# Optimization experiments

Measured on AMD Instinct MI355X. Metric: run time of the kernel, lower is better.

The kernel has to match this reference:

```python
import jax, jax.numpy as jnp
import numpy as np

B, N, H, V = 2048, 16, 512, 780  # trees, nodes per tree, hidden size, vocab size


def _topology():
    """Build one random tree, replicate across B trees, and precompute the
    BFS level schedule on the non-backtracking line graph (as DGL's
    level_order: reversed(edges_back) = up edges leaves-first, then
    edges = down edges root-first)."""
    rng = np.random.default_rng(0)
    parent = np.zeros(N, dtype=np.int64)
    for i in range(1, N):
        parent[i] = rng.integers(0, i)
    depth = np.zeros(N, dtype=np.int64)
    for i in range(1, N):
        depth[i] = depth[parent[i]] + 1
    Epc = 2 * (N - 1)  # directed edges per tree
    src = np.zeros(Epc, dtype=np.int64)
    dst = np.zeros(Epc, dtype=np.int64)
    for i in range(1, N):
        src[2 * (i - 1)] = parent[i]; dst[2 * (i - 1)] = i          # down edge
        src[2 * (i - 1) + 1] = i;     dst[2 * (i - 1) + 1] = parent[i]  # up edge
    # line-graph predecessors of edge e=(u->v): edges f=(w->u) with w != v
    preds = [[f for f in range(Epc) if dst[f] == src[e] and src[f] != dst[e]]
             for e in range(Epc)]
    P = max(1, max(len(p) for p in preds))
    preds_pad = np.full((Epc, P), -1, dtype=np.int64)
    for e, p in enumerate(preds):
        preds_pad[e, :len(p)] = p
    D = int(depth.max())
    levels = []
    for d in range(D, 0, -1):   # upward pass, deepest level first
        levels.append([2 * (i - 1) + 1 for i in range(1, N) if depth[i] == d])
    for d in range(1, D + 1):   # downward pass, root first
        levels.append([2 * (i - 1) for i in range(1, N) if depth[i] == d])
    E = B * Epc                 # index E is the zero dummy row
    offs = np.arange(B, dtype=np.int64) * Epc
    preds_full = np.where(preds_pad[None] >= 0,
                          preds_pad[None] + offs[:, None, None], E)
    preds_full = preds_full.reshape(E, P)
    preds_full = np.concatenate(
        [preds_full, np.full((1, P), E, dtype=np.int64)], axis=0)  # [E+1, P]
    Mmax = max(len(lv) for lv in levels) * B
    lv_arr = np.full((len(levels), Mmax), E, dtype=np.int64)
    for l, lv in enumerate(levels):
        ids = (np.asarray(lv, np.int64)[None] + offs[:, None]).reshape(-1)
        lv_arr[l, :ids.size] = ids
    edge_src = (src[None] + np.arange(B, dtype=np.int64)[:, None] * N).reshape(-1)
    root_children = [2 * (i - 1) + 1 for i in range(1, N) if parent[i] == 0]
    root_in = np.asarray(root_children, np.int64)[None] + offs[:, None]  # [B, R]
    root_nodes = np.arange(B, dtype=np.int64) * N
    return edge_src, preds_full, lv_arr, root_in, root_nodes


def setup_inputs() -> dict:
    key = jax.random.key(0)
    ks = jax.random.split(key, 11)
    edge_src, preds, levels, root_in, root_nodes = _topology()
    s1 = 1.0 / np.sqrt(H)
    s2 = 1.0 / np.sqrt(2 * H)
    return {
        "wid": jax.random.randint(ks[0], (B * N,), 0, V),
        "edge_src": jnp.asarray(edge_src),
        "preds": jnp.asarray(preds),
        "levels": jnp.asarray(levels),
        "root_in": jnp.asarray(root_in),
        "root_nodes": jnp.asarray(root_nodes),
        "emb": jax.random.normal(ks[1], (V, H), jnp.float32),
        "w_r": jax.random.normal(ks[2], (H, H), jnp.float32) * s1,
        "ur_w": jax.random.normal(ks[3], (H, H), jnp.float32) * s1,
        "ur_b": jax.random.normal(ks[4], (H,), jnp.float32) * s1,
        "wz_w": jax.random.normal(ks[5], (2 * H, H), jnp.float32) * s2,
        "wz_b": jax.random.normal(ks[6], (H,), jnp.float32) * s2,
        "wh_w": jax.random.normal(ks[7], (2 * H, H), jnp.float32) * s2,
        "wh_b": jax.random.normal(ks[8], (H,), jnp.float32) * s2,
        "wo_w": jax.random.normal(ks[9], (2 * H, H), jnp.float32) * s2,
        "wo_b": jax.random.normal(ks[10], (H,), jnp.float32) * s2,
    }


def reference(wid, edge_src, preds, levels, root_in, root_nodes,
              emb, w_r, ur_w, ur_b, wz_w, wz_b, wh_w, wh_b, wo_w, wo_b):
    E = edge_src.shape[0]
    Hd = emb.shape[1]
    x = emb[wid]                                           # [B*N, H]
    zero = jnp.zeros((1, Hd), x.dtype)
    sx_all = x[edge_src]                                   # src_x per edge
    src_x = jnp.concatenate([sx_all, zero], axis=0)        # [E+1, H], row E = 0
    src_x_r = jnp.concatenate([sx_all @ w_r, zero], axis=0)  # W_r (no bias)
    h = jnp.zeros((E + 1, Hd), x.dtype)
    for l in range(levels.shape[0]):                       # static BFS levels
        idx = levels[l]                                    # [M], padded with E
        p = preds[idx]                                     # [M, P]
        h_nei = h[p]                                       # [M, P, H]
        sum_h = h_nei.sum(axis=1)
        # GRUMessage: r = sigmoid(dst.src_x_r + U_r(src.h)); m = r * src.h
        r = jax.nn.sigmoid(src_x_r[idx][:, None, :] + h_nei @ ur_w + ur_b)
        sum_g = (r * h_nei).sum(axis=1)
        sx = src_x[idx]
        # GRUUpdate
        z = jax.nn.sigmoid(jnp.concatenate([sx, sum_h], axis=-1) @ wz_w + wz_b)
        pre_h = jnp.tanh(jnp.concatenate([sx, sum_g], axis=-1) @ wh_w + wh_b)
        h = h.at[idx].set((1.0 - z) * sum_h + z * pre_h)
        h = h.at[E].set(0.0)                               # keep dummy row zero
    h_edges = h[:E]                                        # edata['h']
    h_root = h[root_in].sum(axis=1)                        # pull into roots
    x_root = x[root_nodes]
    root_vec = jax.nn.relu(
        jnp.concatenate([x_root, h_root], axis=-1) @ wo_w + wo_b)
    return h_edges, root_vec
```

## Files before the change

kernel.cpp:

```cpp
#include <hip/hip_runtime.h>
#include <hip/hip_bf16.h>
#include <cstddef>

#define HD 512

typedef short s8v __attribute__((ext_vector_type(8)));
typedef short s4v __attribute__((ext_vector_type(4)));
typedef float fx4 __attribute__((ext_vector_type(4)));

#define MFMA(a, b, c) __builtin_amdgcn_mfma_f32_16x16x32_bf16((a), (b), (c), 0, 0, 0)

__device__ __forceinline__ unsigned short f2bf(float f) {
  unsigned int u = __float_as_uint(f);
  unsigned int r = (u + 0x7fffu + ((u >> 16) & 1u)) >> 16;
  return (unsigned short)r;
}
__device__ __forceinline__ float bf2f(unsigned short u) {
  return __uint_as_float(((unsigned int)u) << 16);
}

__device__ __forceinline__ size_t swz_off(int k, int n, int KT) {
  int kt = k >> 5, kr = k & 31;
  int nt = n >> 4, nr = n & 15;
  int lane = ((kr >> 3) << 4) | nr;
  int i = kr & 7;
  return ((((size_t)nt * KT + kt) * 64 + lane) << 3) + i;
}

__global__ void pack_kernel(const float* w_r, const float* ur, const float* wz, const float* wh,
                            const float* wo,
                            unsigned short* W1, unsigned short* WZB, unsigned short* WHB,
                            unsigned short* WUR, unsigned short* WO) {
  int idx = blockIdx.x * blockDim.x + threadIdx.x;
  int stride = gridDim.x * blockDim.x;
  for (int t = idx; t < 512 * 1536; t += stride) {
    int k = t / 1536, n = t - k * 1536;
    float v;
    if (n < 512) v = w_r[k * 512 + n];
    else if (n < 1024) v = wz[k * 512 + (n - 512)];
    else v = wh[k * 512 + (n - 1024)];
    W1[swz_off(k, n, 16)] = f2bf(v);
  }
  for (int t = idx; t < 512 * 512; t += stride) {
    int k = t >> 9, n = t & 511;
    size_t o = swz_off(k, n, 16);
    WZB[o] = f2bf(wz[(512 + k) * 512 + n]);
    WHB[o] = f2bf(wh[(512 + k) * 512 + n]);
    WUR[o] = f2bf(ur[k * 512 + n]);
  }
  for (int t = idx; t < 1024 * 512; t += stride) {
    int k = t >> 9, n = t & 511;
    WO[swz_off(k, n, 32)] = f2bf(wo[k * 512 + n]);
  }
}

__global__ void embed_kernel(const int* wid, const float* emb, unsigned short* x_bf, int BN) {
  int idx = blockIdx.x * blockDim.x + threadIdx.x;
  int stride = gridDim.x * blockDim.x;
  int total = BN * (HD / 8);
  for (int t = idx; t < total; t += stride) {
    int nrow = t >> 6;
    int c8 = (t & 63) << 3;
    int w = wid[nrow];
    const float4* s = (const float4*)(emb + (size_t)w * HD + c8);
    float4 v0 = s[0], v1 = s[1];
    s8v o;
    o[0] = (short)f2bf(v0.x); o[1] = (short)f2bf(v0.y);
    o[2] = (short)f2bf(v0.z); o[3] = (short)f2bf(v0.w);
    o[4] = (short)f2bf(v1.x); o[5] = (short)f2bf(v1.y);
    o[6] = (short)f2bf(v1.z); o[7] = (short)f2bf(v1.w);
    *(s8v*)&x_bf[(size_t)nrow * HD + c8] = o;
  }
}

__global__ void schedule_kernel(const int* preds, int E, int Epc, int P, int* sched) {
  __shared__ int rnd[64];
  int t = threadIdx.x;
  rnd[t] = -1;
  __syncthreads();
  for (int it = 0; it <= Epc; ++it) {
    int newv = -1;
    if (t < Epc && rnd[t] < 0) {
      int mx = 0;
      bool ready = true;
      for (int q = 0; q < P; ++q) {
        int pe = preds[t * P + q];
        if (pe < E) {
          int rp = rnd[pe];
          if (rp < 0) ready = false;
          else if (rp + 1 > mx) mx = rp + 1;
        }
      }
      if (ready) newv = mx;
    }
    __syncthreads();
    if (newv >= 0) rnd[t] = newv;
    __syncthreads();
  }
  if (t == 0) {
    int R = 0;
    for (int e = 0; e < Epc; ++e) if (rnd[e] + 1 > R) R = rnd[e] + 1;
    if (R > 31) R = 31;
    sched[0] = R;
    for (int r = 0; r < 31; ++r) {
      int c = 0;
      if (r < R) {
        for (int e = 0; e < Epc; ++e) if (rnd[e] == r) { sched[33 + r * 32 + c] = e; ++c; }
      }
      sched[1 + r] = c;
    }
  }
}

__global__ __launch_bounds__(512, 4) void gemm_pre_kernel(const unsigned short* x_bf,
                                                          const unsigned short* W1,
                                                          unsigned short* XP, int BN) {
  __shared__ unsigned short lA[2][128 * 72];
  const int nM = BN >> 7;
  const int slab = blockIdx.x / nM;
  const int mt = blockIdx.x - slab * nM;
  const int tid = threadIdx.x, lane = tid & 63, w = tid >> 6;
  const int wm = w & 1, wn = w >> 1;
  const int m0 = mt << 7;
  const int srow = tid >> 2, sc0 = (tid & 3) << 4;
  const int k8 = (lane >> 4) << 3;
  fx4 ac[16];
#pragma unroll
  for (int i = 0; i < 16; i++) { ac[i][0]=0.f; ac[i][1]=0.f; ac[i][2]=0.f; ac[i][3]=0.f; }
  const unsigned short* aptr = x_bf + (size_t)(m0 + srow) * 512 + sc0;
  s8v r0, r1;
  {
    r0 = *(const s8v*)aptr;
    r1 = *(const s8v*)(aptr + 8);
    *(s8v*)&lA[0][srow * 72 + sc0]     = r0;
    *(s8v*)&lA[0][srow * 72 + sc0 + 8] = r1;
    r0 = *(const s8v*)(aptr + 64);
    r1 = *(const s8v*)(aptr + 72);
  }
  for (int ks = 0; ks < 8; ++ks) {
    const int cur = ks & 1;
    __syncthreads();
    if (ks < 7) {
      *(s8v*)&lA[cur ^ 1][srow * 72 + sc0]     = r0;
      *(s8v*)&lA[cur ^ 1][srow * 72 + sc0 + 8] = r1;
    }
    if (ks < 6) {
      const unsigned short* g = aptr + ((ks + 2) << 6);
      r0 = *(const s8v*)g;
      r1 = *(const s8v*)(g + 8);
    }
#pragma unroll
    for (int sub = 0; sub < 2; ++sub) {
      const int kt = (ks << 1) + sub;
      s8v a[4];
#pragma unroll
      for (int mi = 0; mi < 4; ++mi)
        a[mi] = *(const s8v*)&lA[cur][((wm << 6) + (mi << 4) + (lane & 15)) * 72 + (sub << 5) + k8];
#pragma unroll
      for (int ni = 0; ni < 4; ++ni) {
        const int ntile = (slab << 4) + (wn << 2) + ni;
        const s8v b = *(const s8v*)(W1 + ((((size_t)ntile << 4) + kt) * 64 + lane) * 8);
#pragma unroll
        for (int mi = 0; mi < 4; ++mi) ac[mi * 4 + ni] = MFMA(a[mi], b, ac[mi * 4 + ni]);
      }
    }
  }
#pragma unroll
  for (int mi = 0; mi < 4; ++mi) {
#pragma unroll
    for (int q = 0; q < 4; ++q) {
      const int row = (wm << 6) + (mi << 4) + ((lane >> 4) << 2) + q;
#pragma unroll
      for (int ni = 0; ni < 4; ++ni) {
        const int col = (slab << 8) + (wn << 6) + (ni << 4) + (lane & 15);
        XP[(size_t)(m0 + row) * 1536 + col] = f2bf(ac[mi * 4 + ni][q]);
      }
    }
  }
}

struct AP {
  const int* sched;
  const int* preds;
  const int* edge_src;
  const float* ur_b;
  const unsigned short* XP;
  const unsigned short* u_bf_c;
  const unsigned short* hE_c;
  unsigned short* A2h;
  unsigned short* A2g;
  int* eIdx;
  int* srcIdx;
  int B, Epc, P, E;
};

__global__ __launch_bounds__(256) void gatherA_kernel(AP p, int r) {
  const int cnt = p.sched[1 + r];
  if (cnt == 0) return;
  const int M = cnt * p.B;
  const int* lst = p.sched + 33 + r * 32;
  const int lane = threadIdx.x & 63;
  const int waveId = blockIdx.x * 4 + (threadIdx.x >> 6);
  const int totalWaves = gridDim.x * 4;
  for (int m = waveId; m < M; m += totalWaves) {
    const int b = m / cnt;
    const int j = m - b * cnt;
    const int e = b * p.Epc + lst[j];
    const int src = p.edge_src[e];
    if (lane == 0) { p.eIdx[m] = e; p.srcIdx[m] = src; }
    const int c0 = lane << 3;
    const s8v xr8 = *(const s8v*)&p.XP[(size_t)src * 1536 + c0];
    float xb[8], ub[8], sh[8], sg[8];
#pragma unroll
    for (int i = 0; i < 8; i++) {
      xb[i] = bf2f((unsigned short)xr8[i]);
      ub[i] = p.ur_b[c0 + i];
      sh[i] = 0.f; sg[i] = 0.f;
    }
    for (int t = 0; t < p.P; ++t) {
      const int pe = p.preds[(size_t)e * p.P + t];
      if (pe >= p.E) continue;
      const s8v h8 = *(const s8v*)&p.hE_c[(size_t)pe * 512 + c0];
      const s8v u8 = *(const s8v*)&p.u_bf_c[(size_t)pe * 512 + c0];
#pragma unroll
      for (int i = 0; i < 8; i++) {
        const float hv = bf2f((unsigned short)h8[i]);
        const float rr = 1.f / (1.f + __expf(-(xb[i] + bf2f((unsigned short)u8[i]) + ub[i])));
        sh[i] += hv;
        sg[i] += rr * hv;
      }
    }
    s8v shb, sgb;
#pragma unroll
    for (int i = 0; i < 8; i++) { shb[i] = (short)f2bf(sh[i]); sgb[i] = (short)f2bf(sg[i]); }
    *(s8v*)&p.A2h[(size_t)m * 512 + c0] = shb;
    *(s8v*)&p.A2g[(size_t)m * 512 + c0] = sgb;
  }
}

struct BP {
  const int* sched;
  const float* wz_b;
  const float* wh_b;
  const unsigned short* XP;
  const unsigned short* A2h;
  const unsigned short* A2g;
  const unsigned short* WZB;
  const unsigned short* WHB;
  const int* eIdx;
  const int* srcIdx;
  unsigned short* hE;
  int B;
};

__global__ __launch_bounds__(256, 4) void gemmB_kernel(BP p, int r) {
  const int cnt = p.sched[1 + r];
  if (cnt == 0) return;
  const int M = cnt * p.B;
  const int nT = (M >> 5) << 1;
  const int qq = nT >> 3;
  __shared__ unsigned short lZ[2][32 * 72];
  __shared__ unsigned short lH[2][32 * 72];
  __shared__ int eL[32];
  __shared__ int sL[32];
  const int tid = threadIdx.x, lane = tid & 63, w = tid >> 6;
  const int srow = tid >> 3, sc = (tid & 7) << 3;
  const int k8 = (lane >> 4) << 3;

  for (int t0 = blockIdx.x; t0 < nT; t0 += gridDim.x) {
    const int t = (t0 & 7) * qq + (t0 >> 3);
    const int mt = t >> 1, nb = t & 1;
    const int m0 = mt << 5, n0 = nb << 8;
    if (tid < 32) { eL[tid] = p.eIdx[m0 + tid]; sL[tid] = p.srcIdx[m0 + tid]; }
    fx4 aZ[8], aH[8];
#pragma unroll
    for (int i = 0; i < 8; i++) {
      aZ[i][0]=0.f; aZ[i][1]=0.f; aZ[i][2]=0.f; aZ[i][3]=0.f;
      aH[i][0]=0.f; aH[i][1]=0.f; aH[i][2]=0.f; aH[i][3]=0.f;
    }
    const size_t rbase = (size_t)(m0 + srow) * 512 + sc;
    s8v nh, ng;
    {
      *(s8v*)&lZ[0][srow * 72 + sc] = *(const s8v*)&p.A2h[rbase];
      *(s8v*)&lH[0][srow * 72 + sc] = *(const s8v*)&p.A2g[rbase];
      nh = *(const s8v*)&p.A2h[rbase + 64];
      ng = *(const s8v*)&p.A2g[rbase + 64];
    }
    for (int ks = 0; ks < 8; ++ks) {
      const int cur = ks & 1;
      __syncthreads();
      if (ks < 7) {
        *(s8v*)&lZ[cur ^ 1][srow * 72 + sc] = nh;
        *(s8v*)&lH[cur ^ 1][srow * 72 + sc] = ng;
      }
      if (ks < 6) {
        nh = *(const s8v*)&p.A2h[rbase + ((ks + 2) << 6)];
        ng = *(const s8v*)&p.A2g[rbase + ((ks + 2) << 6)];
      }
#pragma unroll
      for (int sub = 0; sub < 2; ++sub) {
        const int kt = (ks << 1) + sub;
        s8v az[2], ah[2];
#pragma unroll
        for (int mi = 0; mi < 2; ++mi) {
          const int ao = ((mi << 4) + (lane & 15)) * 72 + (sub << 5) + k8;
          az[mi] = *(const s8v*)&lZ[cur][ao];
          ah[mi] = *(const s8v*)&lH[cur][ao];
        }
#pragma unroll
        for (int ni = 0; ni < 4; ++ni) {
          const int ntile = (n0 >> 4) + (w << 2) + ni;
          const size_t boff = ((((size_t)ntile << 4) + kt) * 64 + lane) << 3;
          const s8v bz = *(const s8v*)(p.WZB + boff);
          const s8v bh = *(const s8v*)(p.WHB + boff);
#pragma unroll
          for (int mi = 0; mi < 2; ++mi) {
            aZ[mi * 4 + ni] = MFMA(az[mi], bz, aZ[mi * 4 + ni]);
            aH[mi * 4 + ni] = MFMA(ah[mi], bh, aH[mi * 4 + ni]);
          }
        }
      }
    }
#pragma unroll
    for (int mi = 0; mi < 2; ++mi) {
#pragma unroll
      for (int q4 = 0; q4 < 4; ++q4) {
        const int row = (mi << 4) + ((lane >> 4) << 2) + q4;
        const int e = eL[row];
        const int src = sL[row];
#pragma unroll
        for (int ni = 0; ni < 4; ++ni) {
          const int col = n0 + (w << 6) + (ni << 4) + (lane & 15);
          float zpre = aZ[mi * 4 + ni][q4] + bf2f(p.XP[(size_t)src * 1536 + 512 + col]) + p.wz_b[col];
          float hpre = aH[mi * 4 + ni][q4] + bf2f(p.XP[(size_t)src * 1536 + 1024 + col]) + p.wh_b[col];
          float zz = 1.f / (1.f + __expf(-zpre));
          float e2 = __expf(2.f * hpre);
          float th = 1.f - 2.f / (e2 + 1.f);
          float sumh = bf2f(p.A2h[(size_t)(m0 + row) * 512 + col]);
          float hn = (1.f - zz) * sumh + zz * th;
          p.hE[(size_t)e * 512 + col] = f2bf(hn);
        }
      }
    }
    __syncthreads();
  }
}

struct CP {
  const int* sched;
  const unsigned short* hE;
  const unsigned short* WUR;
  const int* eIdx;
  unsigned short* u_bf;
  int B;
};

__global__ __launch_bounds__(256, 4) void gemmC_kernel(CP p, int r) {
  const int cnt = p.sched[1 + r];
  if (cnt == 0) return;
  const int M = cnt * p.B;
  const int nT = (M >> 5) << 1;
  const int qq = nT >> 3;
  __shared__ unsigned short lA[2][32 * 72];
  __shared__ int eL[32];
  const int tid = threadIdx.x, lane = tid & 63, w = tid >> 6;
  const int srow = tid >> 3, sc = (tid & 7) << 3;
  const int k8 = (lane >> 4) << 3;

  for (int t0 = blockIdx.x; t0 < nT; t0 += gridDim.x) {
    const int t = (t0 & 7) * qq + (t0 >> 3);
    const int mt = t >> 1, nb = t & 1;
    const int m0 = mt << 5, n0 = nb << 8;
    if (tid < 32) eL[tid] = p.eIdx[m0 + tid];
    __syncthreads();
    fx4 ac[8];
#pragma unroll
    for (int i = 0; i < 8; i++) { ac[i][0]=0.f; ac[i][1]=0.f; ac[i][2]=0.f; ac[i][3]=0.f; }
    const unsigned short* gbase = p.hE + (size_t)eL[srow] * 512 + sc;
    s8v ra;
    {
      *(s8v*)&lA[0][srow * 72 + sc] = *(const s8v*)gbase;
      ra = *(const s8v*)(gbase + 64);
    }
    for (int ks = 0; ks < 8; ++ks) {
      const int cur = ks & 1;
      __syncthreads();
      if (ks < 7) {
        *(s8v*)&lA[cur ^ 1][srow * 72 + sc] = ra;
      }
      if (ks < 6) {
        ra = *(const s8v*)(gbase + ((ks + 2) << 6));
      }
#pragma unroll
      for (int sub = 0; sub < 2; ++sub) {
        const int kt = (ks << 1) + sub;
        s8v a[2];
#pragma unroll
        for (int mi = 0; mi < 2; ++mi)
          a[mi] = *(const s8v*)&lA[cur][((mi << 4) + (lane & 15)) * 72 + (sub << 5) + k8];
#pragma unroll
        for (int ni = 0; ni < 4; ++ni) {
          const int ntile = (n0 >> 4) + (w << 2) + ni;
          const size_t boff = ((((size_t)ntile << 4) + kt) * 64 + lane) << 3;
          const s8v bu = *(const s8v*)(p.WUR + boff);
#pragma unroll
          for (int mi = 0; mi < 2; ++mi) ac[mi * 4 + ni] = MFMA(a[mi], bu, ac[mi * 4 + ni]);
        }
      }
    }
#pragma unroll
    for (int mi = 0; mi < 2; ++mi) {
#pragma unroll
      for (int q4 = 0; q4 < 4; ++q4) {
        const int row = (mi << 4) + ((lane >> 4) << 2) + q4;
        const int e = eL[row];
#pragma unroll
        for (int ni = 0; ni < 4; ++ni) {
          const int col = n0 + (w << 6) + (ni << 4) + (lane & 15);
          p.u_bf[(size_t)e * 512 + col] = f2bf(ac[mi * 4 + ni][q4]);
        }
      }
    }
    __syncthreads();
  }
}

__global__ void cvt_kernel(const unsigned short* hE, float* h, int total8) {
  int idx = blockIdx.x * blockDim.x + threadIdx.x;
  int stride = gridDim.x * blockDim.x;
  for (int t = idx; t < total8; t += stride) {
    const s8v v = *(const s8v*)&hE[(size_t)t * 8];
    float4 f0 = make_float4(bf2f((unsigned short)v[0]), bf2f((unsigned short)v[1]),
                            bf2f((unsigned short)v[2]), bf2f((unsigned short)v[3]));
    float4 f1 = make_float4(bf2f((unsigned short)v[4]), bf2f((unsigned short)v[5]),
                            bf2f((unsigned short)v[6]), bf2f((unsigned short)v[7]));
    *(float4*)&h[(size_t)t * 8] = f0;
    *(float4*)&h[(size_t)t * 8 + 4] = f1;
  }
}

__global__ void root_gather_kernel(const int* root_nodes, const int* root_in,
                                   const unsigned short* x_bf, const unsigned short* hE,
                                   unsigned short* Aroot, int B, int R0) {
  int lane = threadIdx.x & 63;
  int waveId = blockIdx.x * (blockDim.x >> 6) + (threadIdx.x >> 6);
  int totalWaves = gridDim.x * (blockDim.x >> 6);
  for (int b = waveId; b < B; b += totalWaves) {
    int c0 = lane << 3;
    int nd = root_nodes[b];
    *(s8v*)&Aroot[(size_t)b * 1024 + c0] = *(const s8v*)&x_bf[(size_t)nd * HD + c0];
    float s[8];
#pragma unroll
    for (int i = 0; i < 8; i++) s[i] = 0.f;
    for (int t = 0; t < R0; ++t) {
      int e = root_in[b * R0 + t];
      const s8v h8 = *(const s8v*)&hE[(size_t)e * 512 + c0];
#pragma unroll
      for (int i = 0; i < 8; i++) s[i] += bf2f((unsigned short)h8[i]);
    }
    s8v sb;
#pragma unroll
    for (int i = 0; i < 8; i++) sb[i] = (short)f2bf(s[i]);
    *(s8v*)&Aroot[(size_t)b * 1024 + 512 + c0] = sb;
  }
}

__global__ __launch_bounds__(256) void gemm_root_kernel(const unsigned short* Aroot,
                                                        const unsigned short* WO,
                                                        const float* wo_b, float* out, int B) {
  __shared__ unsigned short lA[32 * 40];
  int tid = threadIdx.x, lane = tid & 63, w = tid >> 6;
  int wm = w & 1, wn = w >> 1;
  int bt = blockIdx.x;
  int mt = bt >> 1, nt = bt & 1;
  int m0 = mt << 5;
  fx4 ac[8];
#pragma unroll
  for (int n = 0; n < 8; n++) { ac[n][0]=0.f; ac[n][1]=0.f; ac[n][2]=0.f; ac[n][3]=0.f; }
  int srow = tid >> 3, squad = tid & 7;
  int arow = (wm << 4) | (lane & 15), k8 = (lane >> 4) << 3;
  for (int kt = 0; kt < 32; ++kt) {
    const unsigned short* g = Aroot + (size_t)(m0 + srow) * 1024 + (kt << 5) + (squad << 2);
    *(s4v*)&lA[srow * 40 + (squad << 2)] = *(const s4v*)g;
    __syncthreads();
    s8v a = *(const s8v*)&lA[arow * 40 + k8];
#pragma unroll
    for (int n = 0; n < 8; n++) {
      int ntile = (nt << 4) + (wn << 3) + n;
      size_t boff = ((((size_t)ntile * 32) + kt) * 64 + lane) << 3;
      ac[n] = MFMA(a, *(const s8v*)(WO + boff), ac[n]);
    }
    __syncthreads();
  }
#pragma unroll
  for (int q = 0; q < 4; q++) {
    int row = (wm << 4) + ((lane >> 4) << 2) + q;
    int m = m0 + row;
#pragma unroll
    for (int n = 0; n < 8; n++) {
      int col = (nt << 8) + (wn << 7) + (n << 4) + (lane & 15);
      float v = ac[n][q] + wo_b[col];
      out[(size_t)m * HD + col] = v > 0.f ? v : 0.f;
    }
  }
}

extern "C" void kernel_launch(void* const* d_in, const int* in_sizes, int n_in,
                              void* d_out, int out_size, void* d_ws, size_t ws_size,
                              hipStream_t stream) {
  const int* wid = (const int*)d_in[0];
  const int* edge_src = (const int*)d_in[1];
  const int* preds = (const int*)d_in[2];
  const int* root_in = (const int*)d_in[4];
  const int* root_nodes = (const int*)d_in[5];
  const float* emb = (const float*)d_in[6];
  const float* w_r = (const float*)d_in[7];
  const float* ur_w = (const float*)d_in[8];
  const float* ur_b = (const float*)d_in[9];
  const float* wz_w = (const float*)d_in[10];
  const float* wz_b = (const float*)d_in[11];
  const float* wh_w = (const float*)d_in[12];
  const float* wh_b = (const float*)d_in[13];
  const float* wo_w = (const float*)d_in[14];
  const float* wo_b = (const float*)d_in[15];

  const int BN = in_sizes[0];
  const int E = in_sizes[1];
  const int Bt = in_sizes[5];
  const int Epc = E / Bt;
  const int P = in_sizes[2] / (E + 1);
  const int R0 = in_sizes[4] / Bt;

  float* h = (float*)d_out;

  char* wp = (char*)d_ws;
  auto alloc = [&](size_t bytes) {
    char* r = wp;
    wp += (bytes + 255) & ~(size_t)255;
    return r;
  };
  unsigned short* x_bf = (unsigned short*)alloc((size_t)BN * 512 * 2);
  unsigned short* XP = (unsigned short*)alloc((size_t)BN * 1536 * 2);
  unsigned short* u_bf = (unsigned short*)alloc((size_t)E * 512 * 2);
  unsigned short* hE = (unsigned short*)alloc((size_t)E * 512 * 2);
  unsigned short* A2h = (unsigned short*)alloc((size_t)E * 512 * 2);
  unsigned short* A2g = (unsigned short*)alloc((size_t)E * 512 * 2);
  int* eIdx = (int*)alloc((size_t)E * 4);
  int* srcIdx = (int*)alloc((size_t)E * 4);
  unsigned short* W1 = (unsigned short*)alloc((size_t)512 * 1536 * 2);
  unsigned short* WZB = (unsigned short*)alloc((size_t)512 * 512 * 2);
  unsigned short* WHB = (unsigned short*)alloc((size_t)512 * 512 * 2);
  unsigned short* WUR = (unsigned short*)alloc((size_t)512 * 512 * 2);
  unsigned short* WO = (unsigned short*)alloc((size_t)1024 * 512 * 2);
  unsigned short* Aroot = (unsigned short*)alloc((size_t)Bt * 1024 * 2);
  int* sched = (int*)alloc(8192);

  hipLaunchKernelGGL(pack_kernel, dim3(512), dim3(256), 0, stream,
                     w_r, ur_w, wz_w, wh_w, wo_w, W1, WZB, WHB, WUR, WO);
  hipLaunchKernelGGL(embed_kernel, dim3(1024), dim3(256), 0, stream, wid, emb, x_bf, BN);
  hipLaunchKernelGGL(schedule_kernel, dim3(1), dim3(64), 0, stream, preds, E, Epc, P, sched);
  hipLaunchKernelGGL(gemm_pre_kernel, dim3((BN / 128) * 6), dim3(512), 0, stream,
                     x_bf, W1, XP, BN);

  AP ap;
  ap.sched = sched; ap.preds = preds; ap.edge_src = edge_src;
  ap.ur_b = ur_b; ap.XP = XP; ap.u_bf_c = u_bf; ap.hE_c = hE;
  ap.A2h = A2h; ap.A2g = A2g; ap.eIdx = eIdx; ap.srcIdx = srcIdx;
  ap.B = Bt; ap.Epc = Epc; ap.P = P; ap.E = E;

  BP bp;
  bp.sched = sched; bp.wz_b = wz_b; bp.wh_b = wh_b;
  bp.XP = XP; bp.A2h = A2h; bp.A2g = A2g;
  bp.WZB = WZB; bp.WHB = WHB;
  bp.eIdx = eIdx; bp.srcIdx = srcIdx;
  bp.hE = hE; bp.B = Bt;

  CP cp;
  cp.sched = sched; cp.hE = hE; cp.WUR = WUR;
  cp.eIdx = eIdx; cp.u_bf = u_bf; cp.B = Bt;

  for (int r = 0; r < Epc && r < 31; ++r) {
    const int g = (r < 16) ? 1024 : 128;
    hipLaunchKernelGGL(gatherA_kernel, dim3(g), dim3(256), 0, stream, ap, r);
    hipLaunchKernelGGL(gemmB_kernel, dim3(g), dim3(256), 0, stream, bp, r);
    hipLaunchKernelGGL(gemmC_kernel, dim3(g), dim3(256), 0, stream, cp, r);
  }

  hipLaunchKernelGGL(cvt_kernel, dim3(2048), dim3(256), 0, stream, hE, h, E * 64);
  hipLaunchKernelGGL(root_gather_kernel, dim3(512), dim3(256), 0, stream,
                     root_nodes, root_in, x_bf, hE, Aroot, Bt, R0);
  hipLaunchKernelGGL(gemm_root_kernel, dim3((Bt / 32) * 2), dim3(256), 0, stream,
                     Aroot, WO, wo_b, h + (size_t)E * 512, Bt);
}
```

Measured before the change: 1.025 ms.

## Double-buffer root GEMM A tiles and reuse B fragments across two M subtiles

Restructures the root output GEMM so each wave computes a 2x4 tile block, reusing each loaded weight fragment for two MFMAs instead of one. A tiles are double-buffered in LDS with a register prefetch of the next 64-wide K chunk, halving barriers per K step. A grid-stride tile loop and occupancy hint are added. This raises register use and only affects a small final stage.

```diff
diff --git a/kernel.cpp b/kernel.cpp
--- a/kernel.cpp
+++ b/kernel.cpp
@@ -465,43 +465,68 @@
   }
 }
 
-__global__ __launch_bounds__(256) void gemm_root_kernel(const unsigned short* Aroot,
-                                                        const unsigned short* WO,
-                                                        const float* wo_b, float* out, int B) {
-  __shared__ unsigned short lA[32 * 40];
-  int tid = threadIdx.x, lane = tid & 63, w = tid >> 6;
-  int wm = w & 1, wn = w >> 1;
-  int bt = blockIdx.x;
-  int mt = bt >> 1, nt = bt & 1;
-  int m0 = mt << 5;
-  fx4 ac[8];
-#pragma unroll
-  for (int n = 0; n < 8; n++) { ac[n][0]=0.f; ac[n][1]=0.f; ac[n][2]=0.f; ac[n][3]=0.f; }
-  int srow = tid >> 3, squad = tid & 7;
-  int arow = (wm << 4) | (lane & 15), k8 = (lane >> 4) << 3;
-  for (int kt = 0; kt < 32; ++kt) {
-    const unsigned short* g = Aroot + (size_t)(m0 + srow) * 1024 + (kt << 5) + (squad << 2);
-    *(s4v*)&lA[srow * 40 + (squad << 2)] = *(const s4v*)g;
+__global__ __launch_bounds__(256, 4) void gemm_root_kernel(const unsigned short* Aroot,
+                                                           const unsigned short* WO,
+                                                           const float* wo_b, float* out, int B) {
+  const int nT = (B >> 5) << 1;
+  __shared__ unsigned short lA[2][32 * 72];
+  const int tid = threadIdx.x, lane = tid & 63, w = tid >> 6;
+  const int srow = tid >> 3, sc = (tid & 7) << 3;
+  const int k8 = (lane >> 4) << 3;
+
+  for (int t = blockIdx.x; t < nT; t += gridDim.x) {
+    const int mt = t >> 1, nb = t & 1;
+    const int m0 = mt << 5, n0 = nb << 8;
+    fx4 ac[8];
+#pragma unroll
+    for (int i = 0; i < 8; i++) { ac[i][0]=0.f; ac[i][1]=0.f; ac[i][2]=0.f; ac[i][3]=0.f; }
+    const unsigned short* gbase = Aroot + (size_t)(m0 + srow) * 1024 + sc;
+    s8v ra;
+    {
+      *(s8v*)&lA[0][srow * 72 + sc] = *(const s8v*)gbase;
+      ra = *(const s8v*)(gbase + 64);
+    }
+    for (int ks = 0; ks < 16; ++ks) {
+      const int cur = ks & 1;
+      __syncthreads();
+      if (ks < 15) {
+        *(s8v*)&lA[cur ^ 1][srow * 72 + sc] = ra;
+      }
+      if (ks < 14) {
+        ra = *(const s8v*)(gbase + ((ks + 2) << 6));
+      }
+#pragma unroll
+      for (int sub = 0; sub < 2; ++sub) {
+        const int kt = (ks << 1) + sub;
+        s8v a[2];
+#pragma unroll
+        for (int mi = 0; mi < 2; ++mi)
+          a[mi] = *(const s8v*)&lA[cur][((mi << 4) + (lane & 15)) * 72 + (sub << 5) + k8];
+#pragma unroll
+        for (int ni = 0; ni < 4; ++ni) {
+          const int ntile = (n0 >> 4) + (w << 2) + ni;
+          const size_t boff = (((size_t)ntile * 32 + kt) * 64 + lane) << 3;
+          const s8v b = *(const s8v*)(WO + boff);
+#pragma unroll
+          for (int mi = 0; mi < 2; ++mi) ac[mi * 4 + ni] = MFMA(a[mi], b, ac[mi * 4 + ni]);
+        }
+      }
+    }
+#pragma unroll
+    for (int mi = 0; mi < 2; ++mi) {
+#pragma unroll
+      for (int q4 = 0; q4 < 4; ++q4) {
+        const int row = (mi << 4) + ((lane >> 4) << 2) + q4;
+        const int m = m0 + row;
+#pragma unroll
+        for (int ni = 0; ni < 4; ++ni) {
+          const int col = n0 + (w << 6) + (ni << 4) + (lane & 15);
+          float v = ac[mi * 4 + ni][q4] + wo_b[col];
+          out[(size_t)m * HD + col] = v > 0.f ? v : 0.f;
+        }
+      }
+    }
     __syncthreads();
-    s8v a = *(const s8v*)&lA[arow * 40 + k8];
-#pragma unroll
-    for (int n = 0; n < 8; n++) {
-      int ntile = (nt << 4) + (wn << 3) + n;
-      size_t boff = ((((size_t)ntile * 32) + kt) * 64 + lane) << 3;
-      ac[n] = MFMA(a, *(const s8v*)(WO + boff), ac[n]);
-    }
-    __syncthreads();
-  }
-#pragma unroll
-  for (int q = 0; q < 4; q++) {
-    int row = (wm << 4) + ((lane >> 4) << 2) + q;
-    int m = m0 + row;
-#pragma unroll
-    for (int n = 0; n < 8; n++) {
-      int col = (nt << 8) + (wn << 7) + (n << 4) + (lane & 15);
-      float v = ac[n][q] + wo_b[col];
-      out[(size_t)m * HD + col] = v > 0.f ? v : 0.f;
-    }
   }
 }
 
```

Result: faster. 944.7 us (-7.9%).
